# Optimization experiments

Measured on AMD Instinct MI355X. Metric: run time of the kernel, lower is better.

## Reference

```python
import jax, jax.numpy as jnp
import numpy as np

HID = 2048; NH = 16; NKV = 2; HD = 128; G = NH // NKV
SEC = (16, 24, 24)  # sums to 64 = HD/2
EPS = 1e-6
B, S = 2, 1024


def _reorder(table):
    # table: [3, B, S, HD]; interleave sections picking axis i%3 per chunk
    chunks = []
    idx = 0
    for _ in range(2):
        for sec in SEC:
            chunks.append(table[..., idx:idx + sec])
            idx += sec
    return jnp.concatenate([c[i % len(SEC)] for i, c in enumerate(chunks)], axis=-1)  # [B,S,HD]


def rotate_half(x):
    x1, x2 = jnp.split(x, 2, axis=-1)
    return jnp.concatenate((-x2, x1), axis=-1)


def rms_norm(x, gamma):
    var = jnp.mean(jnp.square(x), axis=-1, keepdims=True)
    return gamma * (x * jax.lax.rsqrt(var + EPS))


def setup_inputs() -> dict:
    key = jax.random.key(0)
    ks = jax.random.split(key, 12)
    x = jax.random.normal(ks[0], (B, S, HID), dtype=jnp.float32)
    ang = jax.random.uniform(ks[1], (3, B, S, HD), dtype=jnp.float32) * 6.28318
    cos = jnp.cos(ang)
    sin = jnp.sin(ang)
    mask = jnp.ones((B, S), dtype=jnp.float32)
    sc = 0.02
    q_w = jax.random.normal(ks[2], (HID, NH * HD), dtype=jnp.float32) * sc
    q_b = jnp.zeros((NH * HD,), dtype=jnp.float32)
    k_w = jax.random.normal(ks[3], (HID, NKV * HD), dtype=jnp.float32) * sc
    k_b = jnp.zeros((NKV * HD,), dtype=jnp.float32)
    v_w = jax.random.normal(ks[4], (HID, NKV * HD), dtype=jnp.float32) * sc
    v_b = jnp.zeros((NKV * HD,), dtype=jnp.float32)
    q_gamma = jnp.ones((HD,), dtype=jnp.float32)
    k_gamma = jnp.ones((HD,), dtype=jnp.float32)
    o_w = jax.random.normal(ks[5], (NH * HD, HID), dtype=jnp.float32) * sc
    return {"x": x, "cos": cos, "sin": sin, "mask": mask,
            "q_w": q_w, "q_b": q_b, "k_w": k_w, "k_b": k_b,
            "v_w": v_w, "v_b": v_b, "q_gamma": q_gamma, "k_gamma": k_gamma,
            "o_w": o_w}


def reference(x, cos, sin, mask, q_w, q_b, k_w, k_b, v_w, v_b, q_gamma, k_gamma, o_w):
    b, s, _ = x.shape
    # QKV projections
    q = (x @ q_w + q_b).reshape(b, s, NH, HD)
    k = (x @ k_w + k_b).reshape(b, s, NKV, HD)
    v = (x @ v_w + v_b).reshape(b, s, NKV, HD)
    # per-head RMSNorm on q, k
    q = rms_norm(q, q_gamma)
    k = rms_norm(k, k_gamma)
    q = jnp.transpose(q, (0, 2, 1, 3))  # [B,NH,S,HD]
    k = jnp.transpose(k, (0, 2, 1, 3))  # [B,NKV,S,HD]
    v = jnp.transpose(v, (0, 2, 1, 3))
    # multimodal RoPE
    cos_f = _reorder(cos)[:, None, :, :]  # [B,1,S,HD]
    sin_f = _reorder(sin)[:, None, :, :]
    q = q * cos_f + rotate_half(q) * sin_f
    k = k * cos_f + rotate_half(k) * sin_f
    # key-mask zeroing and effective lengths
    eff = mask.sum(axis=-1).astype(jnp.int32)  # [B]
    bm = mask[:, None, :, None]
    k = k * bm
    v = v * bm
    hist = (jnp.arange(s)[None, :] < eff[:, None]).astype(jnp.float32)  # [B,S]
    # GQA attention scores in fp32
    qg = q.reshape(b, NKV, G, s, HD)
    scores = jnp.einsum('bngqd,bnkd->bngqk', qg, k,
                        precision=jax.lax.Precision.HIGHEST) * (HD ** -0.5)
    scores = scores.reshape(b, NH, s, s)
    scores = scores + (1.0 - hist)[:, None, None, :] * -1e9
    causal = jnp.tril(jnp.ones((s, s), dtype=jnp.float32))
    scores = scores + (1.0 - causal)[None, None, :, :] * -1e9
    aw = jax.nn.softmax(scores, axis=-1)
    # weighted values
    out = jnp.einsum('bngqk,bnkd->bngqd', aw.reshape(b, NKV, G, s, s), v,
                     precision=jax.lax.Precision.HIGHEST)
    out = out.reshape(b, NH, s, HD)
    out = jnp.transpose(out, (0, 2, 1, 3)).reshape(b, s, NH * HD)
    return out @ o_w
```

## Files before the change

### kernel.cpp

```cpp
#include <hip/hip_runtime.h>

typedef __attribute__((ext_vector_type(8))) short bf16x8;
typedef __attribute__((ext_vector_type(4))) float f32x4;

#define MFMA16(a, b, c) __builtin_amdgcn_mfma_f32_16x16x32_bf16(a, b, c, 0, 0, 0)

__device__ inline short f2bf(float f) {
  union { float f; unsigned u; } v;
  v.f = f;
  unsigned r = v.u + 0x7FFF + ((v.u >> 16) & 1);
  return (short)(r >> 16);
}
__device__ inline float bf2f(short s) {
  union { unsigned u; float f; } v;
  v.u = ((unsigned)(unsigned short)s) << 16;
  return v.f;
}
#define GLD_LDS16(g, l)                                                        \
  __builtin_amdgcn_global_load_lds(                                            \
      (const __attribute__((address_space(1))) unsigned int*)(g),              \
      (__attribute__((address_space(3))) unsigned int*)(l), 16, 0, 0)

__device__ __forceinline__ void raw_barrier() {
  __asm__ volatile("" ::: "memory");
  __builtin_amdgcn_s_barrier();
  __asm__ volatile("" ::: "memory");
}

__global__ __launch_bounds__(256) void prep_kernel(
    const float* __restrict__ x, const float* __restrict__ q_w,
    const float* __restrict__ k_w, const float* __restrict__ v_w,
    const float* __restrict__ o_w, const float* __restrict__ q_b,
    const float* __restrict__ k_b, const float* __restrict__ v_b,
    short* __restrict__ xb, short* __restrict__ wqkv_t, short* __restrict__ wo_t,
    float* __restrict__ biasAll) {
  __shared__ float t[64][65];
  int bid = blockIdx.x;
  if (bid == 6400) {
    for (int i = threadIdx.x; i < 2560; i += 256) {
      float v = (i < 2048) ? q_b[i] : (i < 2304 ? k_b[i - 2048] : v_b[i - 2304]);
      biasAll[i] = v;
    }
    return;
  }
  if (bid < 4096) {
    int i = (bid * 256 + threadIdx.x) * 4;
    float4 f = *(const float4*)&x[i];
    short4 o;
    o.x = f2bf(f.x); o.y = f2bf(f.y); o.z = f2bf(f.z); o.w = f2bf(f.w);
    *(short4*)&xb[i] = o;
    return;
  }
  bid -= 4096;
  const float* src;
  short* dst;
  int C, bx, by;
  if (bid < 1024) {
    src = q_w; dst = wqkv_t; C = 2048;
    bx = (bid & 31) * 64; by = (bid >> 5) * 64;
  } else if (bid < 1152) {
    bid -= 1024;
    src = k_w; dst = wqkv_t + (size_t)2048 * 2048; C = 256;
    bx = (bid & 3) * 64; by = (bid >> 2) * 64;
  } else if (bid < 1280) {
    bid -= 1152;
    src = v_w; dst = wqkv_t + (size_t)2304 * 2048; C = 256;
    bx = (bid & 3) * 64; by = (bid >> 2) * 64;
  } else {
    bid -= 1280;
    src = o_w; dst = wo_t; C = 2048;
    bx = (bid & 31) * 64; by = (bid >> 5) * 64;
  }
  const int R = 2048;
  const int tx = threadIdx.x & 15;
  const int ty = threadIdx.x >> 4;
#pragma unroll
  for (int i = 0; i < 4; i++) {
    int row = ty + i * 16;
    float4 f = *(const float4*)&src[(size_t)(by + row) * C + bx + tx * 4];
    t[row][tx * 4 + 0] = f.x;
    t[row][tx * 4 + 1] = f.y;
    t[row][tx * 4 + 2] = f.z;
    t[row][tx * 4 + 3] = f.w;
  }
  __syncthreads();
#pragma unroll
  for (int i = 0; i < 4; i++) {
    int c = ty + i * 16;
    short4 o;
    o.x = f2bf(t[tx * 4 + 0][c]);
    o.y = f2bf(t[tx * 4 + 1][c]);
    o.z = f2bf(t[tx * 4 + 2][c]);
    o.w = f2bf(t[tx * 4 + 3][c]);
    *(short4*)&dst[(size_t)(bx + c) * R + by + tx * 4] = o;
  }
}

__global__ __launch_bounds__(256) void gemm_qkv_kernel(const short* __restrict__ A,
                                                       const short* __restrict__ B,
                                                       short* __restrict__ Cs,
                                                       const float* __restrict__ bias,
                                                       int N, int gx, int gy, int P) {
  __shared__ __align__(16) short As[4][64 * 32];
  __shared__ __align__(16) short Bs[4][128 * 32];
  const int bid = blockIdx.x;
  const int xcd = bid & 7, idx = bid >> 3;
  const int colsPerX = gx >> 1, rowsPerX = gy >> 2;
  const int xt = (xcd & 1) * colsPerX + idx % colsPerX;
  const int yt = (xcd >> 1) * rowsPerX + idx / colsPerX;
  const int tid = threadIdx.x;
  const int lane = tid & 63, wave = tid >> 6;
  const int quad = lane >> 4, l16 = lane & 15;
  const int m0 = yt * 64, n0 = xt * 128;
  const int wm = (wave >> 1) * 32, wn = (wave & 1) * 64;
  const int r0 = tid >> 2, c0 = (tid & 3) * 8;
  const int ca = ((tid & 3) ^ ((r0 >> 1) & 3)) * 8;
  const size_t arow = (size_t)(m0 + r0) * 2048;
  const size_t brow0 = (size_t)(n0 + r0) * 2048, brow1 = (size_t)(n0 + r0 + 64) * 2048;
  f32x4 acc[2][4];
#pragma unroll
  for (int mi = 0; mi < 2; mi++)
#pragma unroll
    for (int ni = 0; ni < 4; ni++) acc[mi][ni] = (f32x4){0.f, 0.f, 0.f, 0.f};

#pragma unroll
  for (int st = 0; st < 4; st++) {
    const int kk = st * 32 + ca;
    GLD_LDS16(&A[arow + kk], &As[st][r0 * 32 + c0]);
    GLD_LDS16(&B[brow0 + kk], &Bs[st][r0 * 32 + c0]);
    GLD_LDS16(&B[brow1 + kk], &Bs[st][(r0 + 64) * 32 + c0]);
  }

  const int sx = (l16 >> 1) & 3;
  for (int p = 0; p < P; p++) {
    if (p < P - 1) {
      __asm__ volatile("s_waitcnt vmcnt(6)" ::: "memory");
    } else {
      __asm__ volatile("s_waitcnt vmcnt(0)" ::: "memory");
    }
    raw_barrier();
#pragma unroll
    for (int j = 0; j < 2; j++) {
      const int cur = (2 * p + j) & 3;
      bf16x8 af[2], bfr[4];
#pragma unroll
      for (int mi = 0; mi < 2; mi++)
        af[mi] = *(const bf16x8*)&As[cur][(wm + mi * 16 + l16) * 32 + ((quad ^ sx) * 8)];
#pragma unroll
      for (int ni = 0; ni < 4; ni++)
        bfr[ni] = *(const bf16x8*)&Bs[cur][(wn + ni * 16 + l16) * 32 + ((quad ^ sx) * 8)];
#pragma unroll
      for (int mi = 0; mi < 2; mi++)
#pragma unroll
        for (int ni = 0; ni < 4; ni++)
          acc[mi][ni] = MFMA16(af[mi], bfr[ni], acc[mi][ni]);
    }
    __asm__ volatile("s_waitcnt lgkmcnt(0)" ::: "memory");
    raw_barrier();
    if (p < P - 2) {
#pragma unroll
      for (int j = 0; j < 2; j++) {
        const int st = 2 * p + 4 + j;
        const int slot = st & 3;
        const int kk = st * 32 + ca;
        GLD_LDS16(&A[arow + kk], &As[slot][r0 * 32 + c0]);
        GLD_LDS16(&B[brow0 + kk], &Bs[slot][r0 * 32 + c0]);
        GLD_LDS16(&B[brow1 + kk], &Bs[slot][(r0 + 64) * 32 + c0]);
      }
    }
  }
#pragma unroll
  for (int mi = 0; mi < 2; mi++)
#pragma unroll
    for (int ni = 0; ni < 4; ni++) {
      const int col = n0 + wn + ni * 16 + l16;
      const float bv = bias[col];
#pragma unroll
      for (int r = 0; r < 4; r++)
        Cs[(size_t)(m0 + wm + mi * 16 + quad * 4 + r) * N + col] =
            f2bf(acc[mi][ni][r] + bv);
    }
}

__global__ __launch_bounds__(256) void gemm_db_kernel(const short* __restrict__ A,
                                                      const short* __restrict__ B,
                                                      float* __restrict__ C, int N,
                                                      int gx, int gy, int P) {
  __shared__ __align__(16) short As[4][64 * 32];
  __shared__ __align__(16) short Bs[4][128 * 32];
  const int bid = blockIdx.x;
  const int xcd = bid & 7, idx = bid >> 3;
  const int colsPerX = gx >> 1, rowsPerX = gy >> 2;
  const int xt = (xcd & 1) * colsPerX + idx % colsPerX;
  const int yt = (xcd >> 1) * rowsPerX + idx / colsPerX;
  const int tid = threadIdx.x;
  const int lane = tid & 63, wave = tid >> 6;
  const int quad = lane >> 4, l16 = lane & 15;
  const int m0 = yt * 64, n0 = xt * 128;
  const int wm = (wave >> 1) * 32, wn = (wave & 1) * 64;
  const int r0 = tid >> 2, c0 = (tid & 3) * 8;
  const int ca = ((tid & 3) ^ ((r0 >> 1) & 3)) * 8;
  const size_t arow = (size_t)(m0 + r0) * 2048;
  const size_t brow0 = (size_t)(n0 + r0) * 2048, brow1 = (size_t)(n0 + r0 + 64) * 2048;
  f32x4 acc[2][4];
#pragma unroll
  for (int mi = 0; mi < 2; mi++)
#pragma unroll
    for (int ni = 0; ni < 4; ni++) acc[mi][ni] = (f32x4){0.f, 0.f, 0.f, 0.f};

#pragma unroll
  for (int st = 0; st < 4; st++) {
    const int kk = st * 32 + ca;
    GLD_LDS16(&A[arow + kk], &As[st][r0 * 32 + c0]);
    GLD_LDS16(&B[brow0 + kk], &Bs[st][r0 * 32 + c0]);
    GLD_LDS16(&B[brow1 + kk], &Bs[st][(r0 + 64) * 32 + c0]);
  }

  const int sx = (l16 >> 1) & 3;
  for (int p = 0; p < P; p++) {
    if (p < P - 1) {
      __asm__ volatile("s_waitcnt vmcnt(6)" ::: "memory");
    } else {
      __asm__ volatile("s_waitcnt vmcnt(0)" ::: "memory");
    }
    raw_barrier();
#pragma unroll
    for (int j = 0; j < 2; j++) {
      const int cur = (2 * p + j) & 3;
      bf16x8 af[2], bfr[4];
#pragma unroll
      for (int mi = 0; mi < 2; mi++)
        af[mi] = *(const bf16x8*)&As[cur][(wm + mi * 16 + l16) * 32 + ((quad ^ sx) * 8)];
#pragma unroll
      for (int ni = 0; ni < 4; ni++)
        bfr[ni] = *(const bf16x8*)&Bs[cur][(wn + ni * 16 + l16) * 32 + ((quad ^ sx) * 8)];
#pragma unroll
      for (int mi = 0; mi < 2; mi++)
#pragma unroll
        for (int ni = 0; ni < 4; ni++)
          acc[mi][ni] = MFMA16(af[mi], bfr[ni], acc[mi][ni]);
    }
    __asm__ volatile("s_waitcnt lgkmcnt(0)" ::: "memory");
    raw_barrier();
    if (p < P - 2) {
#pragma unroll
      for (int j = 0; j < 2; j++) {
        const int st = 2 * p + 4 + j;
        const int slot = st & 3;
        const int kk = st * 32 + ca;
        GLD_LDS16(&A[arow + kk], &As[slot][r0 * 32 + c0]);
        GLD_LDS16(&B[brow0 + kk], &Bs[slot][r0 * 32 + c0]);
        GLD_LDS16(&B[brow1 + kk], &Bs[slot][(r0 + 64) * 32 + c0]);
      }
    }
  }
#pragma unroll
  for (int mi = 0; mi < 2; mi++)
#pragma unroll
    for (int ni = 0; ni < 4; ni++)
#pragma unroll
      for (int r = 0; r < 4; r++)
        C[(size_t)(m0 + wm + mi * 16 + quad * 4 + r) * N + n0 + wn + ni * 16 + l16] =
            acc[mi][ni][r];
}

__global__ __launch_bounds__(256) void postv_kernel(
    const short* __restrict__ qkvb, const float* __restrict__ qg,
    const float* __restrict__ kg, const float* __restrict__ cosb,
    const float* __restrict__ sinb, const float* __restrict__ maskp,
    short* __restrict__ qo, short* __restrict__ ko, short* __restrict__ vtb) {
  __shared__ short t[32][33];
  const int bid = blockIdx.x;
  if (bid < 9216) {
    const int rid = bid * 4 + (threadIdx.x >> 6);
    const int lane = threadIdx.x & 63;
    const int slot = rid >> 11;
    const int bs = rid & 2047;
    const int b = bs >> 10, s = bs & 1023;
    const short* row = qkvb + (size_t)bs * 2560;
    int off;
    const float* gamma;
    if (slot < 16) { off = slot * 128; gamma = qg; }
    else { off = 2048 + (slot - 16) * 128; gamma = kg; }
    float v0 = bf2f(row[off + lane]);
    float v1 = bf2f(row[off + 64 + lane]);
    float ss = v0 * v0 + v1 * v1;
#pragma unroll
    for (int o = 1; o < 64; o <<= 1) ss += __shfl_xor(ss, o);
    float r = rsqrtf(ss * (1.0f / 128.0f) + 1e-6f);
    v0 = gamma[lane] * v0 * r;
    v1 = gamma[64 + lane] * v1 * r;
    int sel = (lane < 16) ? 0 : (lane < 40) ? 1 : 2;
    size_t ci = ((size_t)(sel * 2 + b) * 1024 + s) * 128 + lane;
    float c0 = cosb[ci], s0 = sinb[ci], c1 = cosb[ci + 64], s1 = sinb[ci + 64];
    float o0 = v0 * c0 - v1 * s0;
    float o1 = v1 * c1 + v0 * s1;
    if (slot >= 16) { float mk = maskp[bs]; o0 *= mk; o1 *= mk; }
    size_t oidx;
    short* optr;
    if (slot < 16) { oidx = (((size_t)(b * 16 + slot) * 1024) + s) * 128; optr = qo; }
    else { oidx = (((size_t)(b * 2 + (slot - 16)) * 1024) + s) * 128; optr = ko; }
    optr[oidx + lane] = f2bf(o0);
    optr[oidx + 64 + lane] = f2bf(o1);
    return;
  }
  const int b2 = bid - 9216;
  const int d0 = (b2 & 3) * 32;
  const int s0 = ((b2 >> 2) & 31) * 32;
  const int bz = b2 >> 7;
  const int bq = bz >> 1, kv = bz & 1;
  const int tx = threadIdx.x & 31;
  const int ty = threadIdx.x >> 5;
#pragma unroll
  for (int i = 0; i < 4; i++) {
    int s = s0 + ty + i * 8;
    size_t qi = ((size_t)(bq * 1024 + s)) * 2560 + 2304 + kv * 128 + d0 + tx;
    float val = bf2f(qkvb[qi]);
    t[ty + i * 8][tx] = f2bf(val * maskp[bq * 1024 + s]);
  }
  __syncthreads();
#pragma unroll
  for (int i = 0; i < 4; i++)
    vtb[((size_t)bz * 128 + d0 + ty + i * 8) * 1024 + s0 + tx] = t[tx][ty + i * 8];
}

__global__ __launch_bounds__(256) void attn_kernel(const short* __restrict__ Q,
                                                   const short* __restrict__ K,
                                                   const short* __restrict__ Vt_g,
                                                   short* __restrict__ attn) {
  const int qt = 15 - (int)blockIdx.x;
  const int h = blockIdx.y;
  const int b = blockIdx.z;
  const int nsteps = qt + 1;

  const int kv = h >> 3;
  const int tid = threadIdx.x;
  const int wave = tid >> 6, lane = tid & 63;
  const int quad = lane >> 4, l16 = lane & 15;
  __shared__ __align__(16) short Ks[2][64 * 128];
  __shared__ __align__(16) short Vs[2][128 * 64];
  __shared__ __align__(16) short Ps[4][16 * 72];

  const size_t qoff = (((size_t)(b * 16 + h) * 1024) + qt * 64 + wave * 16 + l16) * 128;
  bf16x8 aq[4];
#pragma unroll
  for (int kk = 0; kk < 4; kk++) aq[kk] = *(const bf16x8*)&Q[qoff + kk * 32 + quad * 8];

  f32x4 o[8];
#pragma unroll
  for (int i = 0; i < 8; i++) o[i] = (f32x4){0.f, 0.f, 0.f, 0.f};
  float l[4] = {0.f, 0.f, 0.f, 0.f};
  const int qrow0 = qt * 64 + wave * 16 + quad * 4;
  const size_t koff = ((size_t)(b * 2 + kv) * 1024) * 128;
  const size_t voff = koff;
  const float scale = 0.08838834764831845f;

#define STAGE_KV(bf, ks0)                                                          \
  {                                                                                \
    _Pragma("unroll") for (int it = 0; it < 4; it++) {                             \
      const int c = it * 256 + tid;                                                \
      const int row = c >> 4, sl = c & 15;                                         \
      GLD_LDS16(&K[koff + (size_t)((ks0) + row) * 128 + ((sl ^ (row & 7)) * 8)],   \
                &Ks[bf][c * 8]);                                                   \
      const int d = c >> 3, sv = c & 7;                                            \
      GLD_LDS16(&Vt_g[voff + (size_t)d * 1024 + (ks0) + ((sv ^ (d & 7)) * 8)],     \
                &Vs[bf][c * 8]);                                                   \
    }                                                                              \
  }

  STAGE_KV(0, 0);

  for (int st = 0; st < nsteps; st++) {
    __asm__ volatile("s_waitcnt vmcnt(0)" ::: "memory");
    raw_barrier();
    if (st + 1 < nsteps) { STAGE_KV((st + 1) & 1, (st + 1) * 64); }
    const int cb = st & 1;
    const int ks0 = st * 64;
    f32x4 sc[4];
#pragma unroll
    for (int nt = 0; nt < 4; nt++) sc[nt] = (f32x4){0.f, 0.f, 0.f, 0.f};
    __builtin_amdgcn_s_setprio(1);
#pragma unroll
    for (int nt = 0; nt < 4; nt++) {
      const int rr = nt * 16 + l16;
#pragma unroll
      for (int kk = 0; kk < 4; kk++) {
        bf16x8 bk = *(const bf16x8*)&Ks[cb][rr * 128 + (((kk * 4 + quad) ^ (rr & 7)) * 8)];
        sc[nt] = MFMA16(aq[kk], bk, sc[nt]);
      }
    }
    __builtin_amdgcn_s_setprio(0);
    short* P = &Ps[wave][0];
#pragma unroll
    for (int nt = 0; nt < 4; nt++) {
      const int kcol = ks0 + nt * 16 + l16;
#pragma unroll
      for (int r = 0; r < 4; r++) {
        float p = (kcol > qrow0 + r) ? 0.f : __expf(fmaf(sc[nt][r], scale, -12.0f));
        l[r] += p;
        P[(quad * 4 + r) * 72 + nt * 16 + l16] = f2bf(p);
      }
    }
    __asm__ volatile("s_waitcnt lgkmcnt(0)" ::: "memory");
    bf16x8 pa0 = *(const bf16x8*)&P[l16 * 72 + quad * 8];
    bf16x8 pa1 = *(const bf16x8*)&P[l16 * 72 + 32 + quad * 8];
    __builtin_amdgcn_s_setprio(1);
#pragma unroll
    for (int nt = 0; nt < 8; nt++) {
      const int rr = nt * 16 + l16;
      bf16x8 bv0 = *(const bf16x8*)&Vs[cb][rr * 64 + ((quad ^ (rr & 7)) * 8)];
      bf16x8 bv1 = *(const bf16x8*)&Vs[cb][rr * 64 + (((4 + quad) ^ (rr & 7)) * 8)];
      o[nt] = MFMA16(pa0, bv0, o[nt]);
      o[nt] = MFMA16(pa1, bv1, o[nt]);
    }
    __builtin_amdgcn_s_setprio(0);
  }
#undef STAGE_KV
#pragma unroll
  for (int off = 1; off < 16; off <<= 1)
#pragma unroll
    for (int r = 0; r < 4; r++) l[r] += __shfl_xor(l[r], off);
  float inv[4];
#pragma unroll
  for (int r = 0; r < 4; r++) inv[r] = 1.f / l[r];
  const int lrow = wave * 16 + quad * 4;
  short* dst = attn + ((size_t)(b * 1024 + qt * 64 + lrow)) * 2048 + h * 128;
#pragma unroll
  for (int nt = 0; nt < 8; nt++)
#pragma unroll
    for (int r = 0; r < 4; r++)
      dst[(size_t)r * 2048 + nt * 16 + l16] = f2bf(o[nt][r] * inv[r]);
}

extern "C" void kernel_launch(void* const* d_in, const int* in_sizes, int n_in,
                              void* d_out, int out_size, void* d_ws, size_t ws_size,
                              hipStream_t stream) {
  const float* x = (const float*)d_in[0];
  const float* cosb = (const float*)d_in[1];
  const float* sinb = (const float*)d_in[2];
  const float* mask = (const float*)d_in[3];
  const float* q_w = (const float*)d_in[4];
  const float* q_b = (const float*)d_in[5];
  const float* k_w = (const float*)d_in[6];
  const float* k_b = (const float*)d_in[7];
  const float* v_w = (const float*)d_in[8];
  const float* v_b = (const float*)d_in[9];
  const float* qg = (const float*)d_in[10];
  const float* kg = (const float*)d_in[11];
  const float* o_w = (const float*)d_in[12];
  float* out = (float*)d_out;

  char* ws = (char*)d_ws;
  short* wo_t = (short*)(ws);
  short* wqkv_t = (short*)(ws + ((size_t)8 << 20));
  short* attn = (short*)(ws + ((size_t)9 << 20));
  short* xb = (short*)(ws + ((size_t)18 << 20));
  short* qb = xb;
  short* kb = (short*)(ws + ((size_t)46 << 20));
  short* vtb = (short*)(ws + ((size_t)47 << 20));
  short* qkvb = (short*)(ws + ((size_t)48 << 20));
  float* biasAll = (float*)(ws + ((size_t)68 << 20));

  prep_kernel<<<6401, 256, 0, stream>>>(x, q_w, k_w, v_w, o_w, q_b, k_b, v_b, xb,
                                        wqkv_t, wo_t, biasAll);
  gemm_qkv_kernel<<<640, 256, 0, stream>>>(xb, wqkv_t, qkvb, biasAll, 2560, 20, 32, 32);
  postv_kernel<<<9728, 256, 0, stream>>>(qkvb, qg, kg, cosb, sinb, mask, qb, kb, vtb);
  attn_kernel<<<dim3(16, 16, 2), 256, 0, stream>>>(qb, kb, vtb, attn);
  gemm_db_kernel<<<512, 256, 0, stream>>>(attn, wo_t, out, 2048, 16, 32, 32);
}
```

Before: 222.3 us.

## Fuse QK RMSNorm, RoPE, masking and V transpose into QKV GEMM epilogue

The QKV GEMM epilogue now stages its 64x128 output tile in shared memory and applies per-head RMSNorm, RoPE and key masking for Q/K tiles, or masking plus transpose for V tiles, writing the attention layouts directly. This removes the separate postv kernel launch and the round trip of the bf16 qkv intermediate through global memory. In exchange the GEMM epilogue gains a barrier, a shuffle reduction and scattered cos/sin loads, and the q buffer is moved so it no longer aliases the x buffer that the GEMM reads.

```diff
diff --git a/kernel.cpp b/kernel.cpp
--- a/kernel.cpp
+++ b/kernel.cpp
@@ -96,13 +96,16 @@
   }
 }
 
-__global__ __launch_bounds__(256) void gemm_qkv_kernel(const short* __restrict__ A,
-                                                       const short* __restrict__ B,
-                                                       short* __restrict__ Cs,
-                                                       const float* __restrict__ bias,
-                                                       int N, int gx, int gy, int P) {
-  __shared__ __align__(16) short As[4][64 * 32];
-  __shared__ __align__(16) short Bs[4][128 * 32];
+__global__ __launch_bounds__(256) void gemm_qkv_kernel(
+    const short* __restrict__ A, const short* __restrict__ B,
+    const float* __restrict__ bias, const float* __restrict__ qg,
+    const float* __restrict__ kg, const float* __restrict__ cosb,
+    const float* __restrict__ sinb, const float* __restrict__ maskp,
+    short* __restrict__ qo, short* __restrict__ ko, short* __restrict__ vtb,
+    int gx, int gy, int P) {
+  __shared__ __align__(16) short sm[4 * 64 * 32 + 4 * 128 * 32];
+#define AsP(st) (&sm[(st)*2048])
+#define BsP(st) (&sm[8192 + (st)*4096])
   const int bid = blockIdx.x;
   const int xcd = bid & 7, idx = bid >> 3;
   const int colsPerX = gx >> 1, rowsPerX = gy >> 2;
@@ -126,9 +129,9 @@
 #pragma unroll
   for (int st = 0; st < 4; st++) {
     const int kk = st * 32 + ca;
-    GLD_LDS16(&A[arow + kk], &As[st][r0 * 32 + c0]);
-    GLD_LDS16(&B[brow0 + kk], &Bs[st][r0 * 32 + c0]);
-    GLD_LDS16(&B[brow1 + kk], &Bs[st][(r0 + 64) * 32 + c0]);
+    GLD_LDS16(&A[arow + kk], AsP(st) + r0 * 32 + c0);
+    GLD_LDS16(&B[brow0 + kk], BsP(st) + r0 * 32 + c0);
+    GLD_LDS16(&B[brow1 + kk], BsP(st) + (r0 + 64) * 32 + c0);
   }
 
   const int sx = (l16 >> 1) & 3;
@@ -145,10 +148,10 @@
       bf16x8 af[2], bfr[4];
 #pragma unroll
       for (int mi = 0; mi < 2; mi++)
-        af[mi] = *(const bf16x8*)&As[cur][(wm + mi * 16 + l16) * 32 + ((quad ^ sx) * 8)];
+        af[mi] = *(const bf16x8*)(AsP(cur) + (wm + mi * 16 + l16) * 32 + ((quad ^ sx) * 8));
 #pragma unroll
       for (int ni = 0; ni < 4; ni++)
-        bfr[ni] = *(const bf16x8*)&Bs[cur][(wn + ni * 16 + l16) * 32 + ((quad ^ sx) * 8)];
+        bfr[ni] = *(const bf16x8*)(BsP(cur) + (wn + ni * 16 + l16) * 32 + ((quad ^ sx) * 8));
 #pragma unroll
       for (int mi = 0; mi < 2; mi++)
 #pragma unroll
@@ -163,23 +166,71 @@
         const int st = 2 * p + 4 + j;
         const int slot = st & 3;
         const int kk = st * 32 + ca;
-        GLD_LDS16(&A[arow + kk], &As[slot][r0 * 32 + c0]);
-        GLD_LDS16(&B[brow0 + kk], &Bs[slot][r0 * 32 + c0]);
-        GLD_LDS16(&B[brow1 + kk], &Bs[slot][(r0 + 64) * 32 + c0]);
+        GLD_LDS16(&A[arow + kk], AsP(slot) + r0 * 32 + c0);
+        GLD_LDS16(&B[brow0 + kk], BsP(slot) + r0 * 32 + c0);
+        GLD_LDS16(&B[brow1 + kk], BsP(slot) + (r0 + 64) * 32 + c0);
       }
     }
   }
+  short* Ts = sm;
 #pragma unroll
   for (int mi = 0; mi < 2; mi++)
 #pragma unroll
     for (int ni = 0; ni < 4; ni++) {
-      const int col = n0 + wn + ni * 16 + l16;
-      const float bv = bias[col];
+      const int col = wn + ni * 16 + l16;
+      const float bv = bias[n0 + col];
 #pragma unroll
       for (int r = 0; r < 4; r++)
-        Cs[(size_t)(m0 + wm + mi * 16 + quad * 4 + r) * N + col] =
-            f2bf(acc[mi][ni][r] + bv);
-    }
+        Ts[(wm + mi * 16 + quad * 4 + r) * 136 + col] = f2bf(acc[mi][ni][r] + bv);
+    }
+  __syncthreads();
+
+  if (xt < 18) {
+    const float* gamma = (xt < 16) ? qg : kg;
+    const float g0 = gamma[lane], g1 = gamma[64 + lane];
+    const int sel = (lane < 16) ? 0 : (lane < 40) ? 1 : 2;
+    const bool isK = (xt >= 16);
+#pragma unroll 4
+    for (int i = 0; i < 16; i++) {
+      const int row = wave * 16 + i;
+      const int m = m0 + row;
+      const int bb = m >> 10, s = m & 1023;
+      float v0 = bf2f(Ts[row * 136 + lane]);
+      float v1 = bf2f(Ts[row * 136 + 64 + lane]);
+      float ss = v0 * v0 + v1 * v1;
+#pragma unroll
+      for (int o = 1; o < 64; o <<= 1) ss += __shfl_xor(ss, o);
+      const float rr = rsqrtf(ss * (1.0f / 128.0f) + 1e-6f);
+      v0 = g0 * v0 * rr;
+      v1 = g1 * v1 * rr;
+      const size_t ci = ((size_t)(sel * 2 + bb) * 1024 + s) * 128 + lane;
+      const float c0v = cosb[ci], s0v = sinb[ci];
+      const float c1v = cosb[ci + 64], s1v = sinb[ci + 64];
+      float o0 = v0 * c0v - v1 * s0v;
+      float o1 = v1 * c1v + v0 * s1v;
+      if (isK) { const float mk = maskp[m]; o0 *= mk; o1 *= mk; }
+      short* dst = isK ? ko + (((size_t)(bb * 2 + (xt - 16)) * 1024) + s) * 128
+                       : qo + (((size_t)(bb * 16 + xt) * 1024) + s) * 128;
+      dst[lane] = f2bf(o0);
+      dst[64 + lane] = f2bf(o1);
+    }
+  } else {
+    const int kv = xt - 18;
+    const int d = tid >> 1;
+    const int sb = (tid & 1) * 32;
+    const int bb = m0 >> 10, sg = m0 & 1023;
+    short tmp[32];
+#pragma unroll
+    for (int i = 0; i < 32; i++) {
+      const int srow = sb + i;
+      tmp[i] = f2bf(bf2f(Ts[srow * 136 + d]) * maskp[m0 + srow]);
+    }
+    short* dst = vtb + ((size_t)(bb * 2 + kv) * 128 + d) * 1024 + sg + sb;
+#pragma unroll
+    for (int j = 0; j < 4; j++) *(int4*)&dst[j * 8] = *(const int4*)&tmp[j * 8];
+  }
+#undef AsP
+#undef BsP
 }
 
 __global__ __launch_bounds__(256) void gemm_db_kernel(const short* __restrict__ A,
@@ -264,66 +315,6 @@
             acc[mi][ni][r];
 }
 
-__global__ __launch_bounds__(256) void postv_kernel(
-    const short* __restrict__ qkvb, const float* __restrict__ qg,
-    const float* __restrict__ kg, const float* __restrict__ cosb,
-    const float* __restrict__ sinb, const float* __restrict__ maskp,
-    short* __restrict__ qo, short* __restrict__ ko, short* __restrict__ vtb) {
-  __shared__ short t[32][33];
-  const int bid = blockIdx.x;
-  if (bid < 9216) {
-    const int rid = bid * 4 + (threadIdx.x >> 6);
-    const int lane = threadIdx.x & 63;
-    const int slot = rid >> 11;
-    const int bs = rid & 2047;
-    const int b = bs >> 10, s = bs & 1023;
-    const short* row = qkvb + (size_t)bs * 2560;
-    int off;
-    const float* gamma;
-    if (slot < 16) { off = slot * 128; gamma = qg; }
-    else { off = 2048 + (slot - 16) * 128; gamma = kg; }
-    float v0 = bf2f(row[off + lane]);
-    float v1 = bf2f(row[off + 64 + lane]);
-    float ss = v0 * v0 + v1 * v1;
-#pragma unroll
-    for (int o = 1; o < 64; o <<= 1) ss += __shfl_xor(ss, o);
-    float r = rsqrtf(ss * (1.0f / 128.0f) + 1e-6f);
-    v0 = gamma[lane] * v0 * r;
-    v1 = gamma[64 + lane] * v1 * r;
-    int sel = (lane < 16) ? 0 : (lane < 40) ? 1 : 2;
-    size_t ci = ((size_t)(sel * 2 + b) * 1024 + s) * 128 + lane;
-    float c0 = cosb[ci], s0 = sinb[ci], c1 = cosb[ci + 64], s1 = sinb[ci + 64];
-    float o0 = v0 * c0 - v1 * s0;
-    float o1 = v1 * c1 + v0 * s1;
-    if (slot >= 16) { float mk = maskp[bs]; o0 *= mk; o1 *= mk; }
-    size_t oidx;
-    short* optr;
-    if (slot < 16) { oidx = (((size_t)(b * 16 + slot) * 1024) + s) * 128; optr = qo; }
-    else { oidx = (((size_t)(b * 2 + (slot - 16)) * 1024) + s) * 128; optr = ko; }
-    optr[oidx + lane] = f2bf(o0);
-    optr[oidx + 64 + lane] = f2bf(o1);
-    return;
-  }
-  const int b2 = bid - 9216;
-  const int d0 = (b2 & 3) * 32;
-  const int s0 = ((b2 >> 2) & 31) * 32;
-  const int bz = b2 >> 7;
-  const int bq = bz >> 1, kv = bz & 1;
-  const int tx = threadIdx.x & 31;
-  const int ty = threadIdx.x >> 5;
-#pragma unroll
-  for (int i = 0; i < 4; i++) {
-    int s = s0 + ty + i * 8;
-    size_t qi = ((size_t)(bq * 1024 + s)) * 2560 + 2304 + kv * 128 + d0 + tx;
-    float val = bf2f(qkvb[qi]);
-    t[ty + i * 8][tx] = f2bf(val * maskp[bq * 1024 + s]);
-  }
-  __syncthreads();
-#pragma unroll
-  for (int i = 0; i < 4; i++)
-    vtb[((size_t)bz * 128 + d0 + ty + i * 8) * 1024 + s0 + tx] = t[tx][ty + i * 8];
-}
-
 __global__ __launch_bounds__(256) void attn_kernel(const short* __restrict__ Q,
                                                    const short* __restrict__ K,
                                                    const short* __restrict__ Vt_g,
@@ -455,16 +446,15 @@
   short* wqkv_t = (short*)(ws + ((size_t)8 << 20));
   short* attn = (short*)(ws + ((size_t)9 << 20));
   short* xb = (short*)(ws + ((size_t)18 << 20));
-  short* qb = xb;
   short* kb = (short*)(ws + ((size_t)46 << 20));
   short* vtb = (short*)(ws + ((size_t)47 << 20));
-  short* qkvb = (short*)(ws + ((size_t)48 << 20));
+  short* qb = (short*)(ws + ((size_t)48 << 20));
   float* biasAll = (float*)(ws + ((size_t)68 << 20));
 
   prep_kernel<<<6401, 256, 0, stream>>>(x, q_w, k_w, v_w, o_w, q_b, k_b, v_b, xb,
                                         wqkv_t, wo_t, biasAll);
-  gemm_qkv_kernel<<<640, 256, 0, stream>>>(xb, wqkv_t, qkvb, biasAll, 2560, 20, 32, 32);
-  postv_kernel<<<9728, 256, 0, stream>>>(qkvb, qg, kg, cosb, sinb, mask, qb, kb, vtb);
+  gemm_qkv_kernel<<<640, 256, 0, stream>>>(xb, wqkv_t, biasAll, qg, kg, cosb, sinb, mask,
+                                           qb, kb, vtb, 20, 32, 32);
   attn_kernel<<<dim3(16, 16, 2), 256, 0, stream>>>(qb, kb, vtb, attn);
   gemm_db_kernel<<<512, 256, 0, stream>>>(attn, wo_t, out, 2048, 16, 32, 32);
 }
```

Measured after the change: 225.1 us. No clear change (+1.2%).

## Fuse Q RMSNorm and RoPE into attention kernel prologue

Applied to the files above, without the earlier changes.

Moves the per-head RMSNorm and rotary embedding for Q out of the post-projection kernel and into the attention kernel, which now reads raw Q rows from the QKV buffer and normalizes and rotates them in registers before the QK loop. The post-processing kernel shrinks to handle only K and the V transpose. This removes a full write and re-read of the bf16 Q tensor and most of the post-processing grid. The cost is extra prologue work and cos/sin loads in each attention block, which overlap with the first K/V stage.

```diff
diff --git a/kernel.cpp b/kernel.cpp
--- a/kernel.cpp
+++ b/kernel.cpp
@@ -264,47 +264,39 @@
             acc[mi][ni][r];
 }
 
-__global__ __launch_bounds__(256) void postv_kernel(
-    const short* __restrict__ qkvb, const float* __restrict__ qg,
-    const float* __restrict__ kg, const float* __restrict__ cosb,
-    const float* __restrict__ sinb, const float* __restrict__ maskp,
-    short* __restrict__ qo, short* __restrict__ ko, short* __restrict__ vtb) {
+__global__ __launch_bounds__(256) void postv_kv_kernel(
+    const short* __restrict__ qkvb, const float* __restrict__ kg,
+    const float* __restrict__ cosb, const float* __restrict__ sinb,
+    const float* __restrict__ maskp, short* __restrict__ ko, short* __restrict__ vtb) {
   __shared__ short t[32][33];
   const int bid = blockIdx.x;
-  if (bid < 9216) {
+  if (bid < 1024) {
     const int rid = bid * 4 + (threadIdx.x >> 6);
     const int lane = threadIdx.x & 63;
     const int slot = rid >> 11;
     const int bs = rid & 2047;
     const int b = bs >> 10, s = bs & 1023;
-    const short* row = qkvb + (size_t)bs * 2560;
-    int off;
-    const float* gamma;
-    if (slot < 16) { off = slot * 128; gamma = qg; }
-    else { off = 2048 + (slot - 16) * 128; gamma = kg; }
-    float v0 = bf2f(row[off + lane]);
-    float v1 = bf2f(row[off + 64 + lane]);
+    const short* row = qkvb + (size_t)bs * 2560 + 2048 + slot * 128;
+    float v0 = bf2f(row[lane]);
+    float v1 = bf2f(row[64 + lane]);
     float ss = v0 * v0 + v1 * v1;
 #pragma unroll
     for (int o = 1; o < 64; o <<= 1) ss += __shfl_xor(ss, o);
     float r = rsqrtf(ss * (1.0f / 128.0f) + 1e-6f);
-    v0 = gamma[lane] * v0 * r;
-    v1 = gamma[64 + lane] * v1 * r;
+    v0 = kg[lane] * v0 * r;
+    v1 = kg[64 + lane] * v1 * r;
     int sel = (lane < 16) ? 0 : (lane < 40) ? 1 : 2;
     size_t ci = ((size_t)(sel * 2 + b) * 1024 + s) * 128 + lane;
     float c0 = cosb[ci], s0 = sinb[ci], c1 = cosb[ci + 64], s1 = sinb[ci + 64];
-    float o0 = v0 * c0 - v1 * s0;
-    float o1 = v1 * c1 + v0 * s1;
-    if (slot >= 16) { float mk = maskp[bs]; o0 *= mk; o1 *= mk; }
-    size_t oidx;
-    short* optr;
-    if (slot < 16) { oidx = (((size_t)(b * 16 + slot) * 1024) + s) * 128; optr = qo; }
-    else { oidx = (((size_t)(b * 2 + (slot - 16)) * 1024) + s) * 128; optr = ko; }
-    optr[oidx + lane] = f2bf(o0);
-    optr[oidx + 64 + lane] = f2bf(o1);
+    const float mk = maskp[bs];
+    float o0 = (v0 * c0 - v1 * s0) * mk;
+    float o1 = (v1 * c1 + v0 * s1) * mk;
+    short* dst = ko + (((size_t)(b * 2 + slot) * 1024) + s) * 128;
+    dst[lane] = f2bf(o0);
+    dst[64 + lane] = f2bf(o1);
     return;
   }
-  const int b2 = bid - 9216;
+  const int b2 = bid - 1024;
   const int d0 = (b2 & 3) * 32;
   const int s0 = ((b2 >> 2) & 31) * 32;
   const int bz = b2 >> 7;
@@ -324,10 +316,11 @@
     vtb[((size_t)bz * 128 + d0 + ty + i * 8) * 1024 + s0 + tx] = t[tx][ty + i * 8];
 }
 
-__global__ __launch_bounds__(256) void attn_kernel(const short* __restrict__ Q,
-                                                   const short* __restrict__ K,
-                                                   const short* __restrict__ Vt_g,
-                                                   short* __restrict__ attn) {
+__global__ __launch_bounds__(256) void attn_kernel(
+    const short* __restrict__ qkvb, const short* __restrict__ K,
+    const short* __restrict__ Vt_g, const float* __restrict__ qg,
+    const float* __restrict__ cosb, const float* __restrict__ sinb,
+    short* __restrict__ attn) {
   const int qt = 15 - (int)blockIdx.x;
   const int h = blockIdx.y;
   const int b = blockIdx.z;
@@ -341,16 +334,6 @@
   __shared__ __align__(16) short Vs[2][128 * 64];
   __shared__ __align__(16) short Ps[4][16 * 72];
 
-  const size_t qoff = (((size_t)(b * 16 + h) * 1024) + qt * 64 + wave * 16 + l16) * 128;
-  bf16x8 aq[4];
-#pragma unroll
-  for (int kk = 0; kk < 4; kk++) aq[kk] = *(const bf16x8*)&Q[qoff + kk * 32 + quad * 8];
-
-  f32x4 o[8];
-#pragma unroll
-  for (int i = 0; i < 8; i++) o[i] = (f32x4){0.f, 0.f, 0.f, 0.f};
-  float l[4] = {0.f, 0.f, 0.f, 0.f};
-  const int qrow0 = qt * 64 + wave * 16 + quad * 4;
   const size_t koff = ((size_t)(b * 2 + kv) * 1024) * 128;
   const size_t voff = koff;
   const float scale = 0.08838834764831845f;
@@ -370,6 +353,72 @@
 
   STAGE_KV(0, 0);
 
+  const int s = qt * 64 + wave * 16 + l16;
+  const short* qrow = qkvb + ((size_t)(b * 1024 + s)) * 2560 + h * 128;
+  bf16x8 qraw[4];
+#pragma unroll
+  for (int kk = 0; kk < 4; kk++) qraw[kk] = *(const bf16x8*)&qrow[kk * 32 + quad * 8];
+  float vq[4][8];
+  float ss = 0.f;
+#pragma unroll
+  for (int kk = 0; kk < 4; kk++)
+#pragma unroll
+    for (int e = 0; e < 8; e++) {
+      vq[kk][e] = bf2f(qraw[kk][e]);
+      ss = fmaf(vq[kk][e], vq[kk][e], ss);
+    }
+  ss += __shfl_xor(ss, 16);
+  ss += __shfl_xor(ss, 32);
+  const float rr = rsqrtf(ss * (1.0f / 128.0f) + 1e-6f);
+#pragma unroll
+  for (int kk = 0; kk < 4; kk++) {
+    float4 ga = *(const float4*)&qg[kk * 32 + quad * 8];
+    float4 gb = *(const float4*)&qg[kk * 32 + quad * 8 + 4];
+    vq[kk][0] *= ga.x * rr; vq[kk][1] *= ga.y * rr;
+    vq[kk][2] *= ga.z * rr; vq[kk][3] *= ga.w * rr;
+    vq[kk][4] *= gb.x * rr; vq[kk][5] *= gb.y * rr;
+    vq[kk][6] *= gb.z * rr; vq[kk][7] *= gb.w * rr;
+  }
+  bf16x8 aq[4];
+#pragma unroll
+  for (int kk = 0; kk < 2; kk++) {
+    const int dbase = kk * 32 + quad * 8;
+    const int sel = (dbase < 16) ? 0 : (dbase < 40) ? 1 : 2;
+    const size_t ci = ((size_t)(sel * 2 + b) * 1024 + s) * 128 + dbase;
+    float cd[8], sd[8], cD[8], sD[8];
+    {
+      float4 a0 = *(const float4*)&cosb[ci], a1 = *(const float4*)&cosb[ci + 4];
+      cd[0]=a0.x; cd[1]=a0.y; cd[2]=a0.z; cd[3]=a0.w;
+      cd[4]=a1.x; cd[5]=a1.y; cd[6]=a1.z; cd[7]=a1.w;
+    }
+    {
+      float4 a0 = *(const float4*)&sinb[ci], a1 = *(const float4*)&sinb[ci + 4];
+      sd[0]=a0.x; sd[1]=a0.y; sd[2]=a0.z; sd[3]=a0.w;
+      sd[4]=a1.x; sd[5]=a1.y; sd[6]=a1.z; sd[7]=a1.w;
+    }
+    {
+      float4 a0 = *(const float4*)&cosb[ci + 64], a1 = *(const float4*)&cosb[ci + 68];
+      cD[0]=a0.x; cD[1]=a0.y; cD[2]=a0.z; cD[3]=a0.w;
+      cD[4]=a1.x; cD[5]=a1.y; cD[6]=a1.z; cD[7]=a1.w;
+    }
+    {
+      float4 a0 = *(const float4*)&sinb[ci + 64], a1 = *(const float4*)&sinb[ci + 68];
+      sD[0]=a0.x; sD[1]=a0.y; sD[2]=a0.z; sD[3]=a0.w;
+      sD[4]=a1.x; sD[5]=a1.y; sD[6]=a1.z; sD[7]=a1.w;
+    }
+#pragma unroll
+    for (int e = 0; e < 8; e++) {
+      aq[kk][e] = f2bf(vq[kk][e] * cd[e] - vq[kk + 2][e] * sd[e]);
+      aq[kk + 2][e] = f2bf(vq[kk + 2][e] * cD[e] + vq[kk][e] * sD[e]);
+    }
+  }
+
+  f32x4 o[8];
+#pragma unroll
+  for (int i = 0; i < 8; i++) o[i] = (f32x4){0.f, 0.f, 0.f, 0.f};
+  float l[4] = {0.f, 0.f, 0.f, 0.f};
+  const int qrow0 = qt * 64 + wave * 16 + quad * 4;
+
   for (int st = 0; st < nsteps; st++) {
     __asm__ volatile("s_waitcnt vmcnt(0)" ::: "memory");
     raw_barrier();
@@ -382,10 +431,10 @@
     __builtin_amdgcn_s_setprio(1);
 #pragma unroll
     for (int nt = 0; nt < 4; nt++) {
-      const int rr = nt * 16 + l16;
+      const int rrK = nt * 16 + l16;
 #pragma unroll
       for (int kk = 0; kk < 4; kk++) {
-        bf16x8 bk = *(const bf16x8*)&Ks[cb][rr * 128 + (((kk * 4 + quad) ^ (rr & 7)) * 8)];
+        bf16x8 bk = *(const bf16x8*)&Ks[cb][rrK * 128 + (((kk * 4 + quad) ^ (rrK & 7)) * 8)];
         sc[nt] = MFMA16(aq[kk], bk, sc[nt]);
       }
     }
@@ -407,9 +456,9 @@
     __builtin_amdgcn_s_setprio(1);
 #pragma unroll
     for (int nt = 0; nt < 8; nt++) {
-      const int rr = nt * 16 + l16;
-      bf16x8 bv0 = *(const bf16x8*)&Vs[cb][rr * 64 + ((quad ^ (rr & 7)) * 8)];
-      bf16x8 bv1 = *(const bf16x8*)&Vs[cb][rr * 64 + (((4 + quad) ^ (rr & 7)) * 8)];
+      const int rrV = nt * 16 + l16;
+      bf16x8 bv0 = *(const bf16x8*)&Vs[cb][rrV * 64 + ((quad ^ (rrV & 7)) * 8)];
+      bf16x8 bv1 = *(const bf16x8*)&Vs[cb][rrV * 64 + (((4 + quad) ^ (rrV & 7)) * 8)];
       o[nt] = MFMA16(pa0, bv0, o[nt]);
       o[nt] = MFMA16(pa1, bv1, o[nt]);
     }
@@ -455,7 +504,6 @@
   short* wqkv_t = (short*)(ws + ((size_t)8 << 20));
   short* attn = (short*)(ws + ((size_t)9 << 20));
   short* xb = (short*)(ws + ((size_t)18 << 20));
-  short* qb = xb;
   short* kb = (short*)(ws + ((size_t)46 << 20));
   short* vtb = (short*)(ws + ((size_t)47 << 20));
   short* qkvb = (short*)(ws + ((size_t)48 << 20));
@@ -464,7 +512,7 @@
   prep_kernel<<<6401, 256, 0, stream>>>(x, q_w, k_w, v_w, o_w, q_b, k_b, v_b, xb,
                                         wqkv_t, wo_t, biasAll);
   gemm_qkv_kernel<<<640, 256, 0, stream>>>(xb, wqkv_t, qkvb, biasAll, 2560, 20, 32, 32);
-  postv_kernel<<<9728, 256, 0, stream>>>(qkvb, qg, kg, cosb, sinb, mask, qb, kb, vtb);
-  attn_kernel<<<dim3(16, 16, 2), 256, 0, stream>>>(qb, kb, vtb, attn);
+  postv_kv_kernel<<<1536, 256, 0, stream>>>(qkvb, kg, cosb, sinb, mask, kb, vtb);
+  attn_kernel<<<dim3(16, 16, 2), 256, 0, stream>>>(qkvb, kb, vtb, qg, cosb, sinb, attn);
   gemm_db_kernel<<<512, 256, 0, stream>>>(attn, wo_t, out, 2048, 16, 32, 32);
 }
```

New measurement: 221.2 us, median of 2. No clear change (-0.5%).
